# Kernel tuning notes

Measured on AMD Instinct MI355X. Metric: run time of the kernel, lower is better.

Reference implementation:

```python
import jax, jax.numpy as jnp
import numpy as np

VOCAB, EMB, HID = 32000, 512, 1024
B, T = 16, 128


def setup_inputs() -> dict:
    key = jax.random.key(0)
    ks = jax.random.split(key, 12)
    bound = 1.0 / np.sqrt(HID)
    u = lambda k, shape: jax.random.uniform(k, shape, jnp.float32, -bound, bound)
    return {
        "sentence": jax.random.randint(ks[0], (B, T), 0, VOCAB),
        "emb": jax.random.normal(ks[1], (VOCAB, EMB), jnp.float32),
        "W_i": u(ks[2], (EMB + HID, HID)), "b_i": u(ks[3], (HID,)),
        "W_f": u(ks[4], (EMB + HID, HID)), "b_f": u(ks[5], (HID,)),
        "W_o": u(ks[6], (EMB + HID, HID)), "b_o": u(ks[7], (HID,)),
        "W_c": u(ks[8], (EMB + HID, HID)), "b_c": u(ks[9], (HID,)),
        "W_hq": u(ks[10], (HID, VOCAB)), "b_q": u(ks[11], (VOCAB,)),
    }


def reference(sentence, emb, W_i, b_i, W_f, b_f, W_o, b_o, W_c, b_c, W_hq, b_q):
    # [B,T,E] -> [T,B,E]
    x = jnp.swapaxes(emb[sentence], 0, 1)
    # Fuse the 4 gate matmuls into one concatenated-weight matmul (same math).
    W = jnp.concatenate([W_i, W_f, W_o, W_c], axis=1)  # [E+H, 4H]
    b = jnp.concatenate([b_i, b_f, b_o, b_c])          # [4H]
    h0 = jnp.zeros((x.shape[1], HID), x.dtype)

    def step(carry, xt):
        h, c = carry
        z = jnp.concatenate([xt, h], axis=1) @ W + b   # [B,4H]
        i, f, o, g = jnp.split(z, 4, axis=1)
        i, f, o = jax.nn.sigmoid(i), jax.nn.sigmoid(f), jax.nn.sigmoid(o)
        c = f * c + i * jnp.tanh(g)
        h = o * jnp.tanh(c)
        return (h, c), h

    _, hs = jax.lax.scan(step, (h0, h0), x)            # [T,B,H]
    out = jnp.einsum('tbh,hv->tbv', hs, W_hq) + b_q    # [T,B,V]
    return jnp.transpose(out, (1, 2, 0))               # [B,V,T] as in torch permute(1,2,0)
```

## Files before the change

kernel.cpp:

```cpp
#include <hip/hip_runtime.h>
#include <math.h>

typedef float f32x4 __attribute__((ext_vector_type(4)));
typedef short bf16x8 __attribute__((ext_vector_type(8)));
typedef unsigned int uint4v __attribute__((ext_vector_type(4)));
typedef unsigned short u16;
typedef unsigned int u32;
typedef unsigned long long u64;

#define FLAG_STRIDE 16
#define ACQ_BASE    8192
#define EPOCH_BASE  8448
#define QCNT_BASE   8512
#define TCNT_BASE   8528
#define FLAG_WORDS  ((TCNT_BASE + 1) * FLAG_STRIDE)
#define NTILE       125

__device__ __forceinline__ u16 f2bf(float f) {
    union { float f; unsigned u; } x; x.f = f;
    unsigned r = x.u + 0x7fff + ((x.u >> 16) & 1);
    return (u16)(r >> 16);
}

__device__ __forceinline__ void gload_lds16(const u16* g, u16* l) {
    __builtin_amdgcn_global_load_lds(
        (const __attribute__((address_space(1))) void*)g,
        (__attribute__((address_space(3))) void*)l, 16, 0, 0);
}

__global__ __launch_bounds__(256) void prep(
    const int* __restrict__ sent, const float* __restrict__ emb, u16* __restrict__ xb,
    const float* __restrict__ bi, const float* __restrict__ bf_,
    const float* __restrict__ bo, const float* __restrict__ bc, float* __restrict__ b4,
    const float* __restrict__ Wi, const float* __restrict__ Wf,
    const float* __restrict__ Wo, const float* __restrict__ Wc, u16* __restrict__ wxt) {
    __shared__ float tile[32][33];
    const int bx = blockIdx.x, tid = threadIdx.x;
    if (bx < 1024) {
        int row = bx * 2 + (tid >> 7);
        int t = row >> 4, b = row & 15;
        int idx = sent[b * 128 + t];
        float4 v = ((const float4*)(emb + (size_t)idx * 512))[tid & 127];
        ushort4 s = { f2bf(v.x), f2bf(v.y), f2bf(v.z), f2bf(v.w) };
        ((ushort4*)(xb + (size_t)row * 512))[tid & 127] = s;
        return;
    }
    if (bx < 1040) {
        int i = (bx - 1024) * 256 + tid;
        const float* p = (i < 1024) ? bi : (i < 2048) ? bf_ : (i < 3072) ? bo : bc;
        b4[i] = p[i & 1023];
        return;
    }
    int q = bx - 1040, g = q >> 9, r = q & 511;
    const float* in = (g == 0) ? Wi : (g == 1) ? Wf : (g == 2) ? Wo : Wc;
    u16* out = wxt + (size_t)g * 1024 * 512;
    int rt = (r >> 5) * 32, ct = (r & 31) * 32;
    {
        int rr = tid >> 3, cq = (tid & 7) * 4;
        float4 v = *(const float4*)(in + (size_t)(rt + rr) * 1024 + ct + cq);
        tile[rr][cq] = v.x; tile[rr][cq + 1] = v.y; tile[rr][cq + 2] = v.z; tile[rr][cq + 3] = v.w;
        __syncthreads();
        int c = tid >> 3, rq = (tid & 7) * 4;
        ushort4 s = { f2bf(tile[rq][c]), f2bf(tile[rq + 1][c]),
                      f2bf(tile[rq + 2][c]), f2bf(tile[rq + 3][c]) };
        *(ushort4*)(out + (size_t)(ct + c) * 512 + rt + rq) = s;
    }
}

__global__ __launch_bounds__(256) void gemm_xz(
    const u16* __restrict__ A, const u16* __restrict__ Bt,
    const float* __restrict__ bias, float* __restrict__ C) {
    const int tid = threadIdx.x;
    const int l = tid & 63, w = tid >> 6;
    const int wr = w >> 1, wc = w & 1;
    const int m0 = blockIdx.x * 128, n0 = blockIdx.y * 128;
    const int K = 512;
    __shared__ __align__(16) u16 As[128 * 64];
    __shared__ __align__(16) u16 Bs[128 * 64];
    f32x4 acc[4][4];
    f32x4 zz = { 0.f, 0.f, 0.f, 0.f };
#pragma unroll
    for (int i = 0; i < 4; i++)
#pragma unroll
        for (int j = 0; j < 4; j++) acc[i][j] = zz;
    for (int kt = 0; kt < (K >> 6); ++kt) {
        __syncthreads();
#pragma unroll
        for (int i = 0; i < 4; i++) {
            int cbase = i * 256 + w * 64;
            int c = cbase + l, row = c >> 3, kc = c & 7;
            gload_lds16(A + (size_t)(m0 + row) * K + kt * 64 + kc * 8, As + (size_t)cbase * 8);
            gload_lds16(Bt + (size_t)(n0 + row) * K + kt * 64 + kc * 8, Bs + (size_t)cbase * 8);
        }
        __syncthreads();
#pragma unroll
        for (int kk = 0; kk < 2; kk++) {
            bf16x8 af[4], bfv[4];
#pragma unroll
            for (int mi = 0; mi < 4; mi++)
                af[mi] = *(const bf16x8*)(As + (wr * 64 + mi * 16 + (l & 15)) * 64 + kk * 32 + (l >> 4) * 8);
#pragma unroll
            for (int ni = 0; ni < 4; ni++)
                bfv[ni] = *(const bf16x8*)(Bs + (wc * 64 + ni * 16 + (l & 15)) * 64 + kk * 32 + (l >> 4) * 8);
#pragma unroll
            for (int mi = 0; mi < 4; mi++)
#pragma unroll
                for (int ni = 0; ni < 4; ni++)
                    acc[mi][ni] = __builtin_amdgcn_mfma_f32_16x16x32_bf16(af[mi], bfv[ni], acc[mi][ni], 0, 0, 0);
        }
    }
    const int lr = l >> 4, lc = l & 15;
#pragma unroll
    for (int ni = 0; ni < 4; ni++) {
        int col = n0 + wc * 64 + ni * 16 + lc;
        float bv = bias[col];
#pragma unroll
        for (int mi = 0; mi < 4; mi++)
#pragma unroll
            for (int r = 0; r < 4; r++) {
                int row = m0 + wr * 64 + mi * 16 + lr * 4 + r;
                C[(size_t)row * 4096 + col] = acc[mi][ni][r] + bv;
            }
    }
}

__global__ __launch_bounds__(512, 2) void lstm_proj(
    u16* __restrict__ hs,
    const float* __restrict__ xz,
    const float* __restrict__ Wi, const float* __restrict__ Wf,
    const float* __restrict__ Wo, const float* __restrict__ Wc,
    u32* __restrict__ flags,
    const float* __restrict__ Whq,
    u16* __restrict__ whqt,
    const float* __restrict__ bq, float* __restrict__ out) {
    __shared__ __align__(16) char smem[98816];
    const int bx = blockIdx.x;
    const int tid = threadIdx.x;
    const int w = tid >> 6, l = tid & 63;

    if (tid == 0)
        __hip_atomic_fetch_add(&flags[(size_t)(ACQ_BASE + (bx & 255)) * FLAG_STRIDE], 0u,
                               __ATOMIC_ACQ_REL, __HIP_MEMORY_SCOPE_AGENT);

    if (bx < 64) {
        u16* hstage = (u16*)smem;
        float (*zlds)[16][17] = (float (*)[16][17])(void*)(smem + 32768);
        u32* lds_cnt = (u32*)(smem + 37632);
        const int j = bx;
        const int row = l & 15, hi = l >> 4;
        if (tid == 0) *lds_cnt = 0;

        bf16x8 wf[32];
        if (w < 4) {
            const float* Wg = (w == 0) ? Wi : (w == 1) ? Wf : (w == 2) ? Wo : Wc;
#pragma unroll
            for (int kk = 0; kk < 32; ++kk)
#pragma unroll
                for (int e = 0; e < 8; ++e)
                    wf[kk][e] = f2bf(Wg[(size_t)(512 + kk * 32 + hi * 8 + e) * 1024 + j * 16 + row]);
        }
        __syncthreads();

        const int b = tid >> 4, hc = tid & 15;
        float cst = 0.f;
        float cz0 = 0.f, cz1 = 0.f, cz2 = 0.f, cz3 = 0.f;
        if (tid < 256) {
            const float* xr0 = xz + (size_t)b * 4096 + j * 16 + hc;
            cz0 = xr0[0]; cz1 = xr0[1024]; cz2 = xr0[2048]; cz3 = xr0[3072];
        }

        for (int t = 0; t < 128; ++t) {
            if (t > 0) {
                const u16* hbase = hs + (size_t)(t - 1) * 16 * 1024;
                {
                    int spins = 0;
                    while (true) {
                        u32 f = 1u;
                        if (l < 8)
                            f = __hip_atomic_load(
                                    &flags[(size_t)((t - 1) * 64 + 8 * w + l) * FLAG_STRIDE],
                                    __ATOMIC_RELAXED, __HIP_MEMORY_SCOPE_SYSTEM);
                        if (__ballot(f != 0u) == ~0ull) break;
                        __builtin_amdgcn_s_sleep(1);
                        if (++spins > (1 << 20)) break;
                    }
                }
#pragma unroll
                for (int q = 0; q < 4; ++q) {
                    int jw0 = 8 * w + 2 * q;
                    gload_lds16(hbase + (size_t)((l & 31) >> 1) * 1024
                                      + (jw0 + (l >> 5)) * 16 + (l & 1) * 8,
                                hstage + (size_t)jw0 * 256);
                }
            }
            float nz0 = 0.f, nz1 = 0.f, nz2 = 0.f, nz3 = 0.f;
            if (t < 127 && tid < 256) {
                const float* xr = xz + (size_t)((t + 1) * 16 + b) * 4096 + j * 16 + hc;
                nz0 = xr[0]; nz1 = xr[1024]; nz2 = xr[2048]; nz3 = xr[3072];
            }
            __syncthreads();
            if (t > 0) {
                if (tid == 0)
                    __hip_atomic_store(&flags[(size_t)(EPOCH_BASE + j) * FLAG_STRIDE], (u32)t,
                                       __ATOMIC_RELAXED, __HIP_MEMORY_SCOPE_SYSTEM);
                if (w < 4) {
                    f32x4 zv = { 0.f, 0.f, 0.f, 0.f };
                    f32x4 ac0 = zv, ac1 = zv, ac2 = zv, ac3 = zv;
#pragma unroll
                    for (int kk = 0; kk < 32; kk += 4) {
#pragma unroll
                        for (int u = 0; u < 4; ++u) {
                            int base = (2 * (kk + u) + (hi >> 1)) * 256 + row * 16 + (hi & 1) * 8;
                            bf16x8 a = *(const bf16x8*)(hstage + base);
                            f32x4& ac = (u == 0) ? ac0 : (u == 1) ? ac1 : (u == 2) ? ac2 : ac3;
                            ac = __builtin_amdgcn_mfma_f32_16x16x32_bf16(a, wf[kk + u], ac, 0, 0, 0);
                        }
                    }
                    f32x4 acc = (ac0 + ac1) + (ac2 + ac3);
#pragma unroll
                    for (int r = 0; r < 4; ++r)
                        zlds[w][hi * 4 + r][row] = acc[r];
                }
            }
            __syncthreads();
            if (tid < 256) {
                float zi = cz0, zf = cz1, zo = cz2, zc = cz3;
                if (t > 0) {
                    zi += zlds[0][b][hc]; zf += zlds[1][b][hc];
                    zo += zlds[2][b][hc]; zc += zlds[3][b][hc];
                }
                float ig = 1.f / (1.f + __expf(-zi));
                float fg = 1.f / (1.f + __expf(-zf));
                float og = 1.f / (1.f + __expf(-zo));
                float gg = tanhf(zc);
                cst = fg * cst + ig * gg;
                float h = og * tanhf(cst);
                float hn = __shfl_xor(h, 1);
                u32 pk0 = (u32)f2bf(h) | ((u32)f2bf(hn) << 16);
                u32 p2  = __shfl_xor(pk0, 2);
                u32 p4a = __shfl_xor(pk0, 4);
                u32 p4b = __shfl_xor(p2, 4);
                if (!(l & 7)) {
                    uint4v v = { pk0, p2, p4a, p4b };
                    u16* dst = hs + (size_t)(t * 16 + b) * 1024 + j * 16 + hc;
                    asm volatile("global_store_dwordx4 %0, %1, off sc0 sc1"
                                 :: "v"(dst), "v"(v) : "memory");
                }
                cz0 = nz0; cz1 = nz1; cz2 = nz2; cz3 = nz3;
            }
            if (w < 4) {
                asm volatile("s_waitcnt vmcnt(0)" ::: "memory");
                if (l == 0) {
                    u32 old = atomicAdd(lds_cnt, 1u);
                    if (old == (u32)(4 * t + 3))
                        __hip_atomic_store(&flags[(size_t)(t * 64 + j) * FLAG_STRIDE], 1u,
                                           __ATOMIC_RELAXED, __HIP_MEMORY_SCOPE_SYSTEM);
                }
            }
        }
        if (w == 0) {
            int spins = 0;
            while (true) {
                u32 f = __hip_atomic_load(&flags[(size_t)(127 * 64 + l) * FLAG_STRIDE],
                                          __ATOMIC_RELAXED, __HIP_MEMORY_SCOPE_SYSTEM);
                if (__ballot(f != 0) == ~0ull) break;
                __builtin_amdgcn_s_sleep(1);
                if (++spins > (1 << 20)) break;
            }
            if (l == 0)
                __hip_atomic_store(&flags[(size_t)(EPOCH_BASE + j) * FLAG_STRIDE], 128u,
                                   __ATOMIC_RELAXED, __HIP_MEMORY_SCOPE_SYSTEM);
        }
        return;
    }

    {
        float (*tp)[32][33] = (float (*)[32][33])(void*)smem;
        const int half = tid >> 8, t256 = tid & 255;
        const int r = t256 >> 3, cq = (t256 & 7) * 4;
        const int c = t256 >> 3, rq = (t256 & 7) * 4;
        for (int it = 0; it < 84; ++it) {
            int q = it * 384 + (bx - 64) * 2 + half;
            bool act = q < 32000;
            int rt = 0, ct = 0;
            if (act) { rt = (q / 1000) * 32; ct = (q % 1000) * 32; }
            if (act) {
                float4 v = *(const float4*)(Whq + (size_t)(rt + r) * 32000 + ct + cq);
                tp[half][r][cq] = v.x; tp[half][r][cq + 1] = v.y;
                tp[half][r][cq + 2] = v.z; tp[half][r][cq + 3] = v.w;
            }
            __syncthreads();
            if (act) {
                u64 pk = (u64)f2bf(tp[half][rq][c])
                       | ((u64)f2bf(tp[half][rq + 1][c]) << 16)
                       | ((u64)f2bf(tp[half][rq + 2][c]) << 32)
                       | ((u64)f2bf(tp[half][rq + 3][c]) << 48);
                __hip_atomic_store((u64*)(whqt + (size_t)(ct + c) * 1024 + rt + rq), pk,
                                   __ATOMIC_RELAXED, __HIP_MEMORY_SCOPE_SYSTEM);
            }
            __syncthreads();
        }
        asm volatile("s_waitcnt vmcnt(0)" ::: "memory");
        if (tid == 0)
            __hip_atomic_fetch_add(&flags[(size_t)TCNT_BASE * FLAG_STRIDE], 1u,
                                   __ATOMIC_RELAXED, __HIP_MEMORY_SCOPE_SYSTEM);
    }

    u16* As = (u16*)smem;
    u16* Bs = (u16*)(smem + 32768);
    u32* idx_slot = (u32*)(smem + 98304);
    const int wr = w >> 2, wc = w & 3;
    const int lr = l >> 4, lc = l & 15;

    for (int m = 0; m < 16; ++m) {
        if (w == 0) {
            const u32 need = (u32)(8 * m + 8);
            int spins = 0;
            while (true) {
                u32 e = __hip_atomic_load(&flags[(size_t)(EPOCH_BASE + (bx & 63)) * FLAG_STRIDE],
                                          __ATOMIC_RELAXED, __HIP_MEMORY_SCOPE_SYSTEM);
                u32 tc = 192u;
                if (m == 0)
                    tc = __hip_atomic_load(&flags[(size_t)TCNT_BASE * FLAG_STRIDE],
                                           __ATOMIC_RELAXED, __HIP_MEMORY_SCOPE_SYSTEM);
                if (e >= need && tc >= 192u) break;
                __builtin_amdgcn_s_sleep(8);
                if (++spins > (1 << 20)) break;
            }
        }
        __syncthreads();

        while (true) {
            if (tid == 0)
                *idx_slot = __hip_atomic_fetch_add(&flags[(size_t)(QCNT_BASE + m) * FLAG_STRIDE],
                                                   1u, __ATOMIC_RELAXED, __HIP_MEMORY_SCOPE_AGENT);
            __syncthreads();
            u32 idx = *idx_slot;
            __syncthreads();
            if (idx >= NTILE) break;
            const int n0 = (int)idx * 256;

            auto STAGE = [&](int bi, int kt) {
#pragma unroll
                for (int i = 0; i < 2; ++i) {
                    int C = i * 512 + tid, r = C >> 3, c = C & 7;
                    int sc = c ^ (r & 7);
                    int arow = (8 * m + (r & 7)) * 16 + (r >> 3);
                    gload_lds16(hs + (size_t)arow * 1024 + kt * 64 + sc * 8,
                                As + (size_t)(bi * 8192 + (i * 512 + w * 64) * 8));
                }
#pragma unroll
                for (int i = 0; i < 4; ++i) {
                    int C = i * 512 + tid, r = C >> 3, c = C & 7;
                    int sc = c ^ (r & 7);
                    gload_lds16(whqt + (size_t)(n0 + r) * 1024 + kt * 64 + sc * 8,
                                Bs + (size_t)(bi * 16384 + (i * 512 + w * 64) * 8));
                }
            };

            f32x4 acc[4][4];
            f32x4 zz = { 0.f, 0.f, 0.f, 0.f };
#pragma unroll
            for (int i = 0; i < 4; i++)
#pragma unroll
                for (int jj = 0; jj < 4; jj++) acc[i][jj] = zz;

            int cur = 0;
            STAGE(0, 0);
            __syncthreads();
            for (int kt = 0; kt < 16; ++kt) {
                if (kt + 1 < 16) STAGE(cur ^ 1, kt + 1);
                const u16* Ab = As + cur * 8192;
                const u16* Bb = Bs + cur * 16384;
#pragma unroll
                for (int kk = 0; kk < 2; ++kk) {
                    bf16x8 af[4], bf[4];
#pragma unroll
                    for (int mi = 0; mi < 4; ++mi) {
                        int rA = wr * 64 + mi * 16 + lc;
                        int s = (kk * 4 + lr) ^ (rA & 7);
                        af[mi] = *(const bf16x8*)(Ab + rA * 64 + s * 8);
                    }
#pragma unroll
                    for (int ni = 0; ni < 4; ++ni) {
                        int rB = wc * 64 + ni * 16 + lc;
                        int s = (kk * 4 + lr) ^ (rB & 7);
                        bf[ni] = *(const bf16x8*)(Bb + rB * 64 + s * 8);
                    }
#pragma unroll
                    for (int mi = 0; mi < 4; ++mi)
#pragma unroll
                        for (int ni = 0; ni < 4; ++ni)
                            acc[mi][ni] = __builtin_amdgcn_mfma_f32_16x16x32_bf16(af[mi], bf[ni], acc[mi][ni], 0, 0, 0);
                }
                __syncthreads();
                cur ^= 1;
            }
#pragma unroll
            for (int ni = 0; ni < 4; ni++) {
                int col = n0 + wc * 64 + ni * 16 + lc;
                float bv = bq[col];
#pragma unroll
                for (int mi = 0; mi < 4; mi++) {
                    int r0 = wr * 64 + mi * 16 + lr * 4;
                    int bb = r0 >> 3;
                    int t0 = 8 * m + (r0 & 7);
                    float4 st = { acc[mi][ni][0] + bv, acc[mi][ni][1] + bv,
                                  acc[mi][ni][2] + bv, acc[mi][ni][3] + bv };
                    *(float4*)(out + (size_t)bb * 4096000 + (size_t)col * 128 + t0) = st;
                }
            }
        }
    }
}

extern "C" void kernel_launch(void* const* d_in, const int* in_sizes, int n_in,
                              void* d_out, int out_size, void* d_ws, size_t ws_size,
                              hipStream_t stream) {
    const int*   sent = (const int*)d_in[0];
    const float* emb  = (const float*)d_in[1];
    const float* W_i  = (const float*)d_in[2];
    const float* b_i  = (const float*)d_in[3];
    const float* W_f  = (const float*)d_in[4];
    const float* b_f  = (const float*)d_in[5];
    const float* W_o  = (const float*)d_in[6];
    const float* b_o  = (const float*)d_in[7];
    const float* W_c  = (const float*)d_in[8];
    const float* b_c  = (const float*)d_in[9];
    const float* W_hq = (const float*)d_in[10];
    const float* b_q  = (const float*)d_in[11];
    float* out = (float*)d_out;

    char* ws = (char*)d_ws;
    size_t off = 0;
    auto alloc = [&](size_t bytes) { void* p = ws + off; off += (bytes + 255) & ~255ull; return p; };
    u32*   flags = (u32*)alloc((size_t)FLAG_WORDS * 4);
    float* b4   = (float*)alloc((size_t)4096 * 4);
    u16*   xb   = (u16*)alloc((size_t)2048 * 512 * 2);
    u16*   wxt  = (u16*)alloc((size_t)4096 * 512 * 2);
    u16*   hs   = (u16*)alloc((size_t)2048 * 1024 * 2);
    float* xz   = (float*)alloc((size_t)2048 * 4096 * 4);
    u16*   whqt = (u16*)alloc((size_t)32000 * 1024 * 2);

    hipMemsetAsync(flags, 0, (size_t)FLAG_WORDS * 4, stream);
    prep<<<3088, 256, 0, stream>>>(sent, emb, xb, b_i, b_f, b_o, b_c, b4,
                                   W_i, W_f, W_o, W_c, wxt);
    gemm_xz<<<dim3(16, 32), 256, 0, stream>>>(xb, wxt, b4, xz);
    lstm_proj<<<256, 512, 0, stream>>>(hs, xz, W_i, W_f, W_o, W_c,
                                       flags, W_hq, whqt, b_q, out);
}
```

Measured before the change: 666.8 us.

## Assign each block a fixed output column tile and simplify h stores

The projection phase no longer uses a per-m dynamic work queue. Each block claims one column tile once, waits for the weight transpose to finish, then processes all 16 time-chunks for that tile, so whqt rows stay hot in cache and the per-tile atomic handshake is gone. Blocks whose index is past the 125 tiles exit early, which can leave other blocks idle and unbalanced. The h writes also change from a shuffle-gathered 16-byte store to one 4-byte atomic store per lane pair, which is simpler but issues more, smaller stores.

```diff
diff --git a/kernel.cpp b/kernel.cpp
--- a/kernel.cpp
+++ b/kernel.cpp
@@ -3,7 +3,6 @@
 
 typedef float f32x4 __attribute__((ext_vector_type(4)));
 typedef short bf16x8 __attribute__((ext_vector_type(8)));
-typedef unsigned int uint4v __attribute__((ext_vector_type(4)));
 typedef unsigned short u16;
 typedef unsigned int u32;
 typedef unsigned long long u64;
@@ -236,15 +235,10 @@
                 cst = fg * cst + ig * gg;
                 float h = og * tanhf(cst);
                 float hn = __shfl_xor(h, 1);
-                u32 pk0 = (u32)f2bf(h) | ((u32)f2bf(hn) << 16);
-                u32 p2  = __shfl_xor(pk0, 2);
-                u32 p4a = __shfl_xor(pk0, 4);
-                u32 p4b = __shfl_xor(p2, 4);
-                if (!(l & 7)) {
-                    uint4v v = { pk0, p2, p4a, p4b };
-                    u16* dst = hs + (size_t)(t * 16 + b) * 1024 + j * 16 + hc;
-                    asm volatile("global_store_dwordx4 %0, %1, off sc0 sc1"
-                                 :: "v"(dst), "v"(v) : "memory");
+                if (!(l & 1)) {
+                    unsigned pk = (unsigned)f2bf(h) | ((unsigned)f2bf(hn) << 16);
+                    u32* dst = (u32*)hs + (((size_t)(t * 16 + b) * 1024 + j * 16 + hc) >> 1);
+                    __hip_atomic_store(dst, pk, __ATOMIC_RELAXED, __HIP_MEMORY_SCOPE_SYSTEM);
                 }
                 cz0 = nz0; cz1 = nz1; cz2 = nz2; cz3 = nz3;
             }
@@ -312,103 +306,102 @@
     const int wr = w >> 2, wc = w & 3;
     const int lr = l >> 4, lc = l & 15;
 
+    if (tid == 0)
+        *idx_slot = __hip_atomic_fetch_add(&flags[(size_t)QCNT_BASE * FLAG_STRIDE],
+                                           1u, __ATOMIC_RELAXED, __HIP_MEMORY_SCOPE_AGENT);
+    if (w == 0) {
+        int spins = 0;
+        while (__hip_atomic_load(&flags[(size_t)TCNT_BASE * FLAG_STRIDE],
+                                 __ATOMIC_RELAXED, __HIP_MEMORY_SCOPE_SYSTEM) < 192u) {
+            __builtin_amdgcn_s_sleep(8);
+            if (++spins > (1 << 20)) break;
+        }
+    }
+    __syncthreads();
+    const u32 myIdx = *idx_slot;
+    if (myIdx >= NTILE) return;
+    const int n0 = (int)myIdx * 256;
+
     for (int m = 0; m < 16; ++m) {
         if (w == 0) {
             const u32 need = (u32)(8 * m + 8);
             int spins = 0;
-            while (true) {
-                u32 e = __hip_atomic_load(&flags[(size_t)(EPOCH_BASE + (bx & 63)) * FLAG_STRIDE],
-                                          __ATOMIC_RELAXED, __HIP_MEMORY_SCOPE_SYSTEM);
-                u32 tc = 192u;
-                if (m == 0)
-                    tc = __hip_atomic_load(&flags[(size_t)TCNT_BASE * FLAG_STRIDE],
-                                           __ATOMIC_RELAXED, __HIP_MEMORY_SCOPE_SYSTEM);
-                if (e >= need && tc >= 192u) break;
+            while (__hip_atomic_load(&flags[(size_t)(EPOCH_BASE + (bx & 63)) * FLAG_STRIDE],
+                                     __ATOMIC_RELAXED, __HIP_MEMORY_SCOPE_SYSTEM) < need) {
                 __builtin_amdgcn_s_sleep(8);
                 if (++spins > (1 << 20)) break;
             }
         }
         __syncthreads();
 
-        while (true) {
-            if (tid == 0)
-                *idx_slot = __hip_atomic_fetch_add(&flags[(size_t)(QCNT_BASE + m) * FLAG_STRIDE],
-                                                   1u, __ATOMIC_RELAXED, __HIP_MEMORY_SCOPE_AGENT);
+        auto STAGE = [&](int bi, int kt) {
+#pragma unroll
+            for (int i = 0; i < 2; ++i) {
+                int C = i * 512 + tid, r = C >> 3, c = C & 7;
+                int sc = c ^ (r & 7);
+                int arow = (8 * m + (r & 7)) * 16 + (r >> 3);
+                gload_lds16(hs + (size_t)arow * 1024 + kt * 64 + sc * 8,
+                            As + (size_t)(bi * 8192 + (i * 512 + w * 64) * 8));
+            }
+#pragma unroll
+            for (int i = 0; i < 4; ++i) {
+                int C = i * 512 + tid, r = C >> 3, c = C & 7;
+                int sc = c ^ (r & 7);
+                gload_lds16(whqt + (size_t)(n0 + r) * 1024 + kt * 64 + sc * 8,
+                            Bs + (size_t)(bi * 16384 + (i * 512 + w * 64) * 8));
+            }
+        };
+
+        f32x4 acc[4][4];
+        f32x4 zz = { 0.f, 0.f, 0.f, 0.f };
+#pragma unroll
+        for (int i = 0; i < 4; i++)
+#pragma unroll
+            for (int jj = 0; jj < 4; jj++) acc[i][jj] = zz;
+
+        int cur = 0;
+        STAGE(0, 0);
+        __syncthreads();
+        for (int kt = 0; kt < 16; ++kt) {
+            if (kt + 1 < 16) STAGE(cur ^ 1, kt + 1);
+            const u16* Ab = As + cur * 8192;
+            const u16* Bb = Bs + cur * 16384;
+#pragma unroll
+            for (int kk = 0; kk < 2; ++kk) {
+                bf16x8 af[4], bf[4];
+#pragma unroll
+                for (int mi = 0; mi < 4; ++mi) {
+                    int rA = wr * 64 + mi * 16 + lc;
+                    int s = (kk * 4 + lr) ^ (rA & 7);
+                    af[mi] = *(const bf16x8*)(Ab + rA * 64 + s * 8);
+                }
+#pragma unroll
+                for (int ni = 0; ni < 4; ++ni) {
+                    int rB = wc * 64 + ni * 16 + lc;
+                    int s = (kk * 4 + lr) ^ (rB & 7);
+                    bf[ni] = *(const bf16x8*)(Bb + rB * 64 + s * 8);
+                }
+#pragma unroll
+                for (int mi = 0; mi < 4; ++mi)
+#pragma unroll
+                    for (int ni = 0; ni < 4; ++ni)
+                        acc[mi][ni] = __builtin_amdgcn_mfma_f32_16x16x32_bf16(af[mi], bf[ni], acc[mi][ni], 0, 0, 0);
+            }
             __syncthreads();
-            u32 idx = *idx_slot;
-            __syncthreads();
-            if (idx >= NTILE) break;
-            const int n0 = (int)idx * 256;
-
-            auto STAGE = [&](int bi, int kt) {
-#pragma unroll
-                for (int i = 0; i < 2; ++i) {
-                    int C = i * 512 + tid, r = C >> 3, c = C & 7;
-                    int sc = c ^ (r & 7);
-                    int arow = (8 * m + (r & 7)) * 16 + (r >> 3);
-                    gload_lds16(hs + (size_t)arow * 1024 + kt * 64 + sc * 8,
-                                As + (size_t)(bi * 8192 + (i * 512 + w * 64) * 8));
-                }
-#pragma unroll
-                for (int i = 0; i < 4; ++i) {
-                    int C = i * 512 + tid, r = C >> 3, c = C & 7;
-                    int sc = c ^ (r & 7);
-                    gload_lds16(whqt + (size_t)(n0 + r) * 1024 + kt * 64 + sc * 8,
-                                Bs + (size_t)(bi * 16384 + (i * 512 + w * 64) * 8));
-                }
-            };
-
-            f32x4 acc[4][4];
-            f32x4 zz = { 0.f, 0.f, 0.f, 0.f };
-#pragma unroll
-            for (int i = 0; i < 4; i++)
-#pragma unroll
-                for (int jj = 0; jj < 4; jj++) acc[i][jj] = zz;
-
-            int cur = 0;
-            STAGE(0, 0);
-            __syncthreads();
-            for (int kt = 0; kt < 16; ++kt) {
-                if (kt + 1 < 16) STAGE(cur ^ 1, kt + 1);
-                const u16* Ab = As + cur * 8192;
-                const u16* Bb = Bs + cur * 16384;
-#pragma unroll
-                for (int kk = 0; kk < 2; ++kk) {
-                    bf16x8 af[4], bf[4];
-#pragma unroll
-                    for (int mi = 0; mi < 4; ++mi) {
-                        int rA = wr * 64 + mi * 16 + lc;
-                        int s = (kk * 4 + lr) ^ (rA & 7);
-                        af[mi] = *(const bf16x8*)(Ab + rA * 64 + s * 8);
-                    }
-#pragma unroll
-                    for (int ni = 0; ni < 4; ++ni) {
-                        int rB = wc * 64 + ni * 16 + lc;
-                        int s = (kk * 4 + lr) ^ (rB & 7);
-                        bf[ni] = *(const bf16x8*)(Bb + rB * 64 + s * 8);
-                    }
-#pragma unroll
-                    for (int mi = 0; mi < 4; ++mi)
-#pragma unroll
-                        for (int ni = 0; ni < 4; ++ni)
-                            acc[mi][ni] = __builtin_amdgcn_mfma_f32_16x16x32_bf16(af[mi], bf[ni], acc[mi][ni], 0, 0, 0);
-                }
-                __syncthreads();
-                cur ^= 1;
-            }
-#pragma unroll
-            for (int ni = 0; ni < 4; ni++) {
-                int col = n0 + wc * 64 + ni * 16 + lc;
-                float bv = bq[col];
-#pragma unroll
-                for (int mi = 0; mi < 4; mi++) {
-                    int r0 = wr * 64 + mi * 16 + lr * 4;
-                    int bb = r0 >> 3;
-                    int t0 = 8 * m + (r0 & 7);
-                    float4 st = { acc[mi][ni][0] + bv, acc[mi][ni][1] + bv,
-                                  acc[mi][ni][2] + bv, acc[mi][ni][3] + bv };
-                    *(float4*)(out + (size_t)bb * 4096000 + (size_t)col * 128 + t0) = st;
-                }
+            cur ^= 1;
+        }
+#pragma unroll
+        for (int ni = 0; ni < 4; ni++) {
+            int col = n0 + wc * 64 + ni * 16 + lc;
+            float bv = bq[col];
+#pragma unroll
+            for (int mi = 0; mi < 4; mi++) {
+                int r0 = wr * 64 + mi * 16 + lr * 4;
+                int bb = r0 >> 3;
+                int t0 = 8 * m + (r0 & 7);
+                float4 st = { acc[mi][ni][0] + bv, acc[mi][ni][1] + bv,
+                              acc[mi][ni][2] + bv, acc[mi][ni][3] + bv };
+                *(float4*)(out + (size_t)bb * 4096000 + (size_t)col * 128 + t0) = st;
             }
         }
     }
```

New measurement: 657.0 us. About the same (-1.5%).
